# Performance work log

Hardware: AMD Instinct MI355X
Metric: run time of the kernel (lower is better)

The kernel has to match this reference:

```python
import jax, jax.numpy as jnp
import numpy as np

# sparse_shape = grid_size[::-1] + [1,0,0] for grid_size=[1408,1600,40]
Z, Y, X = 41, 1600, 1408
N = 400000
CIN, COUT = 4, 16
EPS = 1e-3  # BatchNorm1d eps from partial(nn.BatchNorm1d, eps=0.001)


def setup_inputs() -> dict:
    # unique active voxel coordinates (submanifold conv assumes no duplicates)
    rng = np.random.default_rng(0)
    pool = Z * Y * X
    raw = rng.integers(0, pool, size=3 * N, dtype=np.int64)
    lin = np.unique(raw)[:N]
    assert lin.size == N
    z = lin // (Y * X)
    rem = lin % (Y * X)
    y = rem // X
    x = rem % X
    coords = np.stack([np.zeros(N, np.int64), z, y, x], axis=1).astype(np.int32)

    key = jax.random.key(0)
    k1, k2 = jax.random.split(key)
    voxel_features = jax.random.normal(k1, (N, CIN), dtype=jnp.float32)
    # SubMConv3d weight: one [CIN,COUT] matrix per kernel offset (27 = 3^3)
    weight = jax.random.normal(k2, (27, CIN, COUT), dtype=jnp.float32) * 0.1
    gamma = jnp.ones((COUT,), dtype=jnp.float32)
    beta = jnp.zeros((COUT,), dtype=jnp.float32)
    return {
        "voxel_features": voxel_features,
        "voxel_coords": jnp.asarray(coords),
        "weight": weight,
        "gamma": gamma,
        "beta": beta,
    }


_OFFSETS = jnp.asarray(
    np.stack(np.meshgrid([-1, 0, 1], [-1, 0, 1], [-1, 0, 1], indexing="ij"), -1
             ).reshape(27, 3),
    dtype=jnp.int32,
)


def _subm_conv(feats, coords, weight):
    """Submanifold sparse 3D conv: outputs only at active voxel sites.

    Rulebook built via sorted linear keys + searchsorted (gather-GEMM).
    """
    zyx = coords[:, 1:4].astype(jnp.int32)                 # [N,3]
    keys = (zyx[:, 0] * Y + zyx[:, 1]) * X + zyx[:, 2]     # [N] unique linear key
    order = jnp.argsort(keys)
    skeys = keys[order]

    nb = zyx[None, :, :] + _OFFSETS[:, None, :]            # [27,N,3]
    inb = ((nb >= 0).all(-1)
           & (nb[..., 0] < Z) & (nb[..., 1] < Y) & (nb[..., 2] < X))
    nkeys = (nb[..., 0] * Y + nb[..., 1]) * X + nb[..., 2]  # [27,N]
    pos = jnp.clip(jnp.searchsorted(skeys, nkeys), 0, N - 1)
    found = inb & (skeys[pos] == nkeys)                    # neighbor is active
    idx = order[pos]                                       # [27,N] row into feats

    gathered = jnp.where(found[..., None], feats[idx], 0.0)  # [27,N,CIN]
    return jnp.einsum("knc,kco->no", gathered, weight)       # [N,COUT]


def reference(voxel_features, voxel_coords, weight, gamma, beta):
    out = _subm_conv(voxel_features, voxel_coords, weight)
    # BatchNorm1d in training mode: normalize over the N (voxel) axis
    mu = out.mean(0)
    var = out.var(0)
    out = (out - mu) * jax.lax.rsqrt(var + EPS) * gamma + beta
    return jax.nn.relu(out)
```

## Files before the change

### kernel.cpp

```cpp
#include <hip/hip_runtime.h>
#include <hip/hip_cooperative_groups.h>
#include <stdint.h>

namespace cg = cooperative_groups;

#define ZD 41
#define YD 1600
#define XD 1408
#define YXD (YD * XD)
#define NKEYS (ZD * YD * XD)
#define ENT_WORDS (NKEYS / 32)
#define BN_EPS 1e-3f

typedef unsigned long long u64;


__global__ void __launch_bounds__(256, 7) fused_all(
    const float4* __restrict__ feats, const int4* __restrict__ coords,
    const float* __restrict__ weight, const float* __restrict__ gamma,
    const float* __restrict__ beta, u64* __restrict__ entry,
    float* __restrict__ partial, float* __restrict__ partial2,
    float* __restrict__ out, int n, int nb, float invN) {
  cg::grid_group grid = cg::this_grid();
  const int tid = threadIdx.x;

  __shared__ float wl[27 * 64];
  __shared__ float swred[4][32];
  __shared__ float red2[8][32];
  __shared__ float redv[32];
  __shared__ float sa[16], sbv[16];

  {
    int ia = blockIdx.x * 256 + tid;
    int4 cl = coords[n - 1];
    int glast = ((cl.y * YD + cl.z) * XD + cl.w) >> 5;
    int stride = gridDim.x * 256;
    for (int g = glast + 1 + ia; g < ENT_WORDS; g += stride)
      entry[g] = (u64)(uint32_t)n;
    if (ia < n) {
      int4 c = coords[ia];
      int key = (c.y * YD + c.z) * XD + c.w;
      int g = key >> 5;
      int pkey = __shfl_up(key, 1);
      if ((tid & 63) == 0 && ia > 0) {
        int4 cp = coords[ia - 1];
        pkey = (cp.y * YD + cp.z) * XD + cp.w;
      }
      int pg = (ia > 0) ? (pkey >> 5) : -1;
      if (g != pg) {
        for (int gg = pg + 1; gg < g; ++gg) entry[gg] = (u64)(uint32_t)ia;
        uint32_t bits = 1u << (key & 31);
        int j = ia + 1;
        while (j < n) {
          int4 cj = coords[j];
          int kj = (cj.y * YD + cj.z) * XD + cj.w;
          if ((kj >> 5) != g) break;
          bits |= 1u << (kj & 31);
          ++j;
        }
        entry[g] = ((u64)bits << 32) | (uint32_t)ia;
      }
    }
  }
  __threadfence();
  grid.sync();

  for (int t = tid; t < 27 * 64; t += 256) wl[t] = weight[t];
  __syncthreads();

  int B = gridDim.x;
  int q = B >> 3, r = B & 7;
  int xcd = blockIdx.x & 7, off = blockIdx.x >> 3;
  int sbk = (xcd < r ? xcd * (q + 1) : r * (q + 1) + (xcd - r) * q) + off;
  int i = sbk * 256 + tid;

  float acc[16];
#pragma unroll
  for (int o = 0; o < 16; o++) acc[o] = 0.f;

  if (i < n) {
    int4 czyx = coords[i];
    int z = czyx.y, y = czyx.z, x = czyx.w;
    int key = (z * YD + y) * XD + x;

    {
      float4 fs = feats[i];
      const float* wp = &wl[13 * 64];
#pragma unroll
      for (int o = 0; o < 16; o++)
        acc[o] = fs.x * wp[o] + fs.y * wp[o + 16] + fs.z * wp[o + 32] +
                 fs.w * wp[o + 48];
    }

    unsigned mask27 = 0;
#pragma unroll
    for (int dzy = 0; dzy < 9; dzy++) {
      const int dz = dzy / 3 - 1, dy = dzy % 3 - 1;
      bool ok = ((unsigned)(z + dz) < (unsigned)ZD) &&
                ((unsigned)(y + dy) < (unsigned)YD);
      int base = key + dz * YXD + dy * XD - 1;
      int g0 = base >> 5;
      u64 e0 = 0, e1 = 0;
      if (ok) {
        e0 = entry[g0];
        e1 = entry[g0 + 1];
      }
      u64 W = (e0 >> 32) | (e1 & 0xFFFFFFFF00000000ull);
      unsigned m3 = (unsigned)(W >> (base & 31)) & 7u;
      mask27 |= m3 << (dzy * 3);
    }
    mask27 &= ~(1u << 13);
    if (x == 0) mask27 &= ~0x1249249u;
    if (x == XD - 1) mask27 &= ~0x4924924u;

    while (mask27) {
      int b = __ffs(mask27) - 1;
      mask27 &= mask27 - 1;
      int dzy = (b * 11) >> 5;
      int rem = b - dzy * 3;
      int dzq = (dzy * 11) >> 5;
      int dyr = dzy - dzq * 3;
      int s = key + (dzq - 1) * YXD + (dyr - 1) * XD + rem - 1;
      int gs = s >> 5;
      u64 e = entry[gs];
      int j = (int)(e & 0xFFFFFFFFull) +
              __popc((uint32_t)(e >> 32) & ((1u << (s & 31)) - 1u));
      float4 f = feats[j];
      const float* wp = &wl[b * 64];
#pragma unroll
      for (int o = 0; o < 16; o++)
        acc[o] += f.x * wp[o] + f.y * wp[o + 16] + f.z * wp[o + 32] +
                  f.w * wp[o + 48];
    }
  }

  {
    int lane = tid & 63, wv = tid >> 6;
#pragma unroll
    for (int o = 0; o < 16; o++) {
      float s = acc[o], qq = acc[o] * acc[o];
#pragma unroll
      for (int offx = 32; offx; offx >>= 1) {
        s += __shfl_xor(s, offx);
        qq += __shfl_xor(qq, offx);
      }
      if (lane == 0) {
        swred[wv][o] = s;
        swred[wv][16 + o] = qq;
      }
    }
    __syncthreads();
    if (tid < 32) {
      float v = swred[0][tid] + swred[1][tid] + swred[2][tid] + swred[3][tid];
      partial[(size_t)blockIdx.x * 32 + tid] = v;
    }
  }
  __threadfence();
  grid.sync();

  if (blockIdx.x < 64) {
    int c = tid & 31, s = tid >> 5;
    float v = 0.f;
    for (int rr = blockIdx.x + 64 * s; rr < nb; rr += 512)
      v += partial[(size_t)rr * 32 + c];
    red2[s][c] = v;
    __syncthreads();
    if (tid < 32) {
      float vv = 0.f;
#pragma unroll
      for (int k = 0; k < 8; k++) vv += red2[k][tid];
      partial2[(size_t)blockIdx.x * 32 + tid] = vv;
    }
  }
  __threadfence();
  grid.sync();

  {
    int c = tid & 31, s = tid >> 5;
    float v = 0.f;
#pragma unroll
    for (int k = 0; k < 8; k++) v += partial2[(size_t)(s + 8 * k) * 32 + c];
    red2[s][c] = v;
    __syncthreads();
    if (tid < 32) {
      float vv = 0.f;
#pragma unroll
      for (int k = 0; k < 8; k++) vv += red2[k][tid];
      redv[tid] = vv;
    }
    __syncthreads();
    if (tid < 16) {
      float mu = redv[tid] * invN;
      float var = redv[16 + tid] * invN - mu * mu;
      float inv = rsqrtf(var + BN_EPS);
      float a = gamma[tid] * inv;
      sa[tid] = a;
      sbv[tid] = beta[tid] - mu * a;
    }
    __syncthreads();
    if (i < n) {
      float4* o4 = (float4*)(out + (size_t)i * 16);
      float4 t0, t1, t2, t3;
      t0.x = fmaxf(acc[0] * sa[0] + sbv[0], 0.f);
      t0.y = fmaxf(acc[1] * sa[1] + sbv[1], 0.f);
      t0.z = fmaxf(acc[2] * sa[2] + sbv[2], 0.f);
      t0.w = fmaxf(acc[3] * sa[3] + sbv[3], 0.f);
      t1.x = fmaxf(acc[4] * sa[4] + sbv[4], 0.f);
      t1.y = fmaxf(acc[5] * sa[5] + sbv[5], 0.f);
      t1.z = fmaxf(acc[6] * sa[6] + sbv[6], 0.f);
      t1.w = fmaxf(acc[7] * sa[7] + sbv[7], 0.f);
      t2.x = fmaxf(acc[8] * sa[8] + sbv[8], 0.f);
      t2.y = fmaxf(acc[9] * sa[9] + sbv[9], 0.f);
      t2.z = fmaxf(acc[10] * sa[10] + sbv[10], 0.f);
      t2.w = fmaxf(acc[11] * sa[11] + sbv[11], 0.f);
      t3.x = fmaxf(acc[12] * sa[12] + sbv[12], 0.f);
      t3.y = fmaxf(acc[13] * sa[13] + sbv[13], 0.f);
      t3.z = fmaxf(acc[14] * sa[14] + sbv[14], 0.f);
      t3.w = fmaxf(acc[15] * sa[15] + sbv[15], 0.f);
      o4[0] = t0;
      o4[1] = t1;
      o4[2] = t2;
      o4[3] = t3;
    }
  }
}

__global__ void __launch_bounds__(256) build_index(
    const int4* __restrict__ coords, u64* __restrict__ entry, int n) {
  int i = blockIdx.x * blockDim.x + threadIdx.x;
  {
    int4 cl = coords[n - 1];
    int glast = (((cl.y * YD + cl.z) * XD + cl.w)) >> 5;
    int stride = gridDim.x * blockDim.x;
    for (int g = glast + 1 + i; g < ENT_WORDS; g += stride)
      entry[g] = (u64)(uint32_t)n;
  }
  if (i >= n) return;
  int4 c = coords[i];
  int key = (c.y * YD + c.z) * XD + c.w;
  int g = key >> 5;
  int pkey = __shfl_up(key, 1);
  if ((threadIdx.x & 63) == 0 && i > 0) {
    int4 cp = coords[i - 1];
    pkey = (cp.y * YD + cp.z) * XD + cp.w;
  }
  int pg = (i > 0) ? (pkey >> 5) : -1;
  if (g != pg) {
    for (int gg = pg + 1; gg < g; ++gg) entry[gg] = (u64)(uint32_t)i;
    uint32_t bits = 1u << (key & 31);
    int j = i + 1;
    while (j < n) {
      int4 cj = coords[j];
      int kj = (cj.y * YD + cj.z) * XD + cj.w;
      if ((kj >> 5) != g) break;
      bits |= 1u << (kj & 31);
      ++j;
    }
    entry[g] = ((u64)bits << 32) | (uint32_t)i;
  }
}

__global__ void __launch_bounds__(256) subm_conv(
    const float4* __restrict__ feats, const int4* __restrict__ coords,
    const float* __restrict__ weight, const u64* __restrict__ entry,
    float* __restrict__ out, float* __restrict__ partial, int n) {
  __shared__ float wl[27 * 64];
  __shared__ float swred[4][32];
  for (int t = threadIdx.x; t < 27 * 64; t += 256) wl[t] = weight[t];
  __syncthreads();
  int B = gridDim.x;
  int q = B >> 3, r = B & 7;
  int xcd = blockIdx.x & 7, off = blockIdx.x >> 3;
  int sb = (xcd < r ? xcd * (q + 1) : r * (q + 1) + (xcd - r) * q) + off;
  int i = sb * 256 + (int)threadIdx.x;
  float acc[16];
#pragma unroll
  for (int o = 0; o < 16; o++) acc[o] = 0.f;
  if (i < n) {
    int4 czyx = coords[i];
    int z = czyx.y, y = czyx.z, x = czyx.w;
    int key = (z * YD + y) * XD + x;
    {
      float4 fs = feats[i];
      const float* wp = &wl[13 * 64];
#pragma unroll
      for (int o = 0; o < 16; o++)
        acc[o] = fs.x * wp[o] + fs.y * wp[o + 16] + fs.z * wp[o + 32] +
                 fs.w * wp[o + 48];
    }
    unsigned mask27 = 0;
#pragma unroll
    for (int dzy = 0; dzy < 9; dzy++) {
      const int dz = dzy / 3 - 1, dy = dzy % 3 - 1;
      bool ok = ((unsigned)(z + dz) < (unsigned)ZD) &&
                ((unsigned)(y + dy) < (unsigned)YD);
      int base = key + dz * YXD + dy * XD - 1;
      int g0 = base >> 5;
      u64 e0 = 0, e1 = 0;
      if (ok) {
        e0 = entry[g0];
        e1 = entry[g0 + 1];
      }
      u64 W = (e0 >> 32) | (e1 & 0xFFFFFFFF00000000ull);
      unsigned m3 = (unsigned)(W >> (base & 31)) & 7u;
      mask27 |= m3 << (dzy * 3);
    }
    mask27 &= ~(1u << 13);
    if (x == 0) mask27 &= ~0x1249249u;
    if (x == XD - 1) mask27 &= ~0x4924924u;
    while (mask27) {
      int b = __ffs(mask27) - 1;
      mask27 &= mask27 - 1;
      int dzy = (b * 11) >> 5;
      int rem = b - dzy * 3;
      int dzq = (dzy * 11) >> 5;
      int dyr = dzy - dzq * 3;
      int s = key + (dzq - 1) * YXD + (dyr - 1) * XD + rem - 1;
      int gs = s >> 5;
      u64 e = entry[gs];
      int j = (int)(e & 0xFFFFFFFFull) +
              __popc((uint32_t)(e >> 32) & ((1u << (s & 31)) - 1u));
      float4 f = feats[j];
      const float* wp = &wl[b * 64];
#pragma unroll
      for (int o = 0; o < 16; o++)
        acc[o] += f.x * wp[o] + f.y * wp[o + 16] + f.z * wp[o + 32] +
                  f.w * wp[o + 48];
    }
    float4* o4 = (float4*)(out + (size_t)i * 16);
    o4[0] = make_float4(acc[0], acc[1], acc[2], acc[3]);
    o4[1] = make_float4(acc[4], acc[5], acc[6], acc[7]);
    o4[2] = make_float4(acc[8], acc[9], acc[10], acc[11]);
    o4[3] = make_float4(acc[12], acc[13], acc[14], acc[15]);
  }
  int lane = threadIdx.x & 63, wv = threadIdx.x >> 6;
#pragma unroll
  for (int o = 0; o < 16; o++) {
    float s = acc[o], qq = acc[o] * acc[o];
#pragma unroll
    for (int offx = 32; offx; offx >>= 1) {
      s += __shfl_xor(s, offx);
      qq += __shfl_xor(qq, offx);
    }
    if (lane == 0) {
      swred[wv][o] = s;
      swred[wv][16 + o] = qq;
    }
  }
  __syncthreads();
  if (threadIdx.x < 32) {
    float v = swred[0][threadIdx.x] + swred[1][threadIdx.x] +
              swred[2][threadIdx.x] + swred[3][threadIdx.x];
    partial[(size_t)blockIdx.x * 32 + threadIdx.x] = v;
  }
}

__global__ void __launch_bounds__(1024) bn_finalize(
    const float4* __restrict__ partial4, float* __restrict__ accum, int nb) {
  __shared__ float4 s4[1024];
  int t = threadIdx.x;
  int q = t & 7;
  int row0 = t >> 3;
  float4 v = make_float4(0.f, 0.f, 0.f, 0.f);
  for (int b = row0; b < nb; b += 128) {
    float4 p = partial4[(size_t)b * 8 + q];
    v.x += p.x;
    v.y += p.y;
    v.z += p.z;
    v.w += p.w;
  }
  s4[t] = v;
  __syncthreads();
  for (int half = 64; half >= 1; half >>= 1) {
    if (row0 < half) {
      float4 o = s4[t + half * 8];
      v.x += o.x;
      v.y += o.y;
      v.z += o.z;
      v.w += o.w;
      s4[t] = v;
    }
    __syncthreads();
  }
  if (t < 8) ((float4*)accum)[t] = s4[t];
}

__global__ void __launch_bounds__(256) bn_apply(
    float* __restrict__ out, const float* __restrict__ accum,
    const float* __restrict__ gamma, const float* __restrict__ beta, int n4,
    float invN) {
  __shared__ float sa[16], sb[16];
  int t = threadIdx.x;
  if (t < 16) {
    float mu = accum[t] * invN;
    float var = accum[16 + t] * invN - mu * mu;
    float inv = rsqrtf(var + BN_EPS);
    float a = gamma[t] * inv;
    sa[t] = a;
    sb[t] = beta[t] - mu * a;
  }
  __syncthreads();
  int i = blockIdx.x * 256 + t;
  if (i >= n4) return;
  float4* p = (float4*)out;
  float4 v = p[i];
  int c0 = (i & 3) * 4;
  v.x = fmaxf(v.x * sa[c0 + 0] + sb[c0 + 0], 0.f);
  v.y = fmaxf(v.y * sa[c0 + 1] + sb[c0 + 1], 0.f);
  v.z = fmaxf(v.z * sa[c0 + 2] + sb[c0 + 2], 0.f);
  v.w = fmaxf(v.w * sa[c0 + 3] + sb[c0 + 3], 0.f);
  p[i] = v;
}

extern "C" void kernel_launch(void* const* d_in, const int* in_sizes, int n_in,
                              void* d_out, int out_size, void* d_ws,
                              size_t ws_size, hipStream_t stream) {
  const float4* feats = (const float4*)d_in[0];
  const int4* coords = (const int4*)d_in[1];
  const float* weight = (const float*)d_in[2];
  const float* gamma = (const float*)d_in[3];
  const float* beta = (const float*)d_in[4];
  int n = in_sizes[0] / 4;

  float* accum = (float*)d_ws;
  u64* entry = (u64*)((char*)d_ws + 256);
  float* partial = (float*)((char*)d_ws + 256 + (size_t)ENT_WORDS * 8 + 16);
  int nb = (n + 255) / 256;
  float* partial2 = partial + (size_t)nb * 32;
  float* out = (float*)d_out;
  float invN = 1.0f / n;

  int maxB = 0, numCU = 0;
  hipOccupancyMaxActiveBlocksPerMultiprocessor(&maxB, fused_all, 256, 0);
  hipDeviceGetAttribute(&numCU, hipDeviceAttributeMultiprocessorCount, 0);

  if ((long)maxB * numCU >= nb) {
    void* args[] = {(void*)&feats, (void*)&coords,  (void*)&weight,
                    (void*)&gamma, (void*)&beta,    (void*)&entry,
                    (void*)&partial, (void*)&partial2, (void*)&out,
                    (void*)&n,     (void*)&nb,      (void*)&invN};
    hipLaunchCooperativeKernel((void*)fused_all, dim3(nb), dim3(256), args, 0,
                               stream);
  } else {
    hipLaunchKernelGGL(build_index, dim3(nb), dim3(256), 0, stream, coords,
                       entry, n);
    hipLaunchKernelGGL(subm_conv, dim3(nb), dim3(256), 0, stream, feats,
                       coords, weight, entry, out, partial, n);
    hipLaunchKernelGGL(bn_finalize, dim3(1), dim3(1024), 0, stream,
                       (const float4*)partial, accum, nb);
    int n4 = n * 4;
    hipLaunchKernelGGL(bn_apply, dim3((n4 + 255) / 256), dim3(256), 0, stream,
                       out, accum, gamma, beta, n4, invN);
  }
}
```

Measured before the change: 124.3 us.

## Fix cooperative grid at 1024 blocks with two voxels per thread

```diff
diff --git a/kernel.cpp b/kernel.cpp
--- a/kernel.cpp
+++ b/kernel.cpp
@@ -11,126 +11,135 @@
 #define NKEYS (ZD * YD * XD)
 #define ENT_WORDS (NKEYS / 32)
 #define BN_EPS 1e-3f
+#define GRIDB 1024
+#define TOT (GRIDB * 256)
 
 typedef unsigned long long u64;
 
 
-__global__ void __launch_bounds__(256, 7) fused_all(
+__global__ void __launch_bounds__(256, 4) fused_all(
     const float4* __restrict__ feats, const int4* __restrict__ coords,
     const float* __restrict__ weight, const float* __restrict__ gamma,
     const float* __restrict__ beta, u64* __restrict__ entry,
     float* __restrict__ partial, float* __restrict__ partial2,
-    float* __restrict__ out, int n, int nb, float invN) {
+    float* __restrict__ out, int n, float invN) {
   cg::grid_group grid = cg::this_grid();
   const int tid = threadIdx.x;
 
-  __shared__ float wl[27 * 64];
+  __shared__ float wl[27 * 68];
   __shared__ float swred[4][32];
   __shared__ float red2[8][32];
   __shared__ float redv[32];
   __shared__ float sa[16], sbv[16];
 
   {
-    int ia = blockIdx.x * 256 + tid;
     int4 cl = coords[n - 1];
     int glast = ((cl.y * YD + cl.z) * XD + cl.w) >> 5;
-    int stride = gridDim.x * 256;
-    for (int g = glast + 1 + ia; g < ENT_WORDS; g += stride)
+    int base = blockIdx.x * 256 + tid;
+    for (int g = glast + 1 + base; g < ENT_WORDS; g += TOT)
       entry[g] = (u64)(uint32_t)n;
-    if (ia < n) {
-      int4 c = coords[ia];
-      int key = (c.y * YD + c.z) * XD + c.w;
-      int g = key >> 5;
-      int pkey = __shfl_up(key, 1);
-      if ((tid & 63) == 0 && ia > 0) {
-        int4 cp = coords[ia - 1];
-        pkey = (cp.y * YD + cp.z) * XD + cp.w;
-      }
-      int pg = (ia > 0) ? (pkey >> 5) : -1;
-      if (g != pg) {
-        for (int gg = pg + 1; gg < g; ++gg) entry[gg] = (u64)(uint32_t)ia;
-        uint32_t bits = 1u << (key & 31);
-        int j = ia + 1;
-        while (j < n) {
-          int4 cj = coords[j];
-          int kj = (cj.y * YD + cj.z) * XD + cj.w;
-          if ((kj >> 5) != g) break;
-          bits |= 1u << (kj & 31);
-          ++j;
+#pragma unroll
+    for (int pass = 0; pass < 2; pass++) {
+      int ia = pass * TOT + base;
+      if (ia < n) {
+        int4 c = coords[ia];
+        int key = (c.y * YD + c.z) * XD + c.w;
+        int g = key >> 5;
+        int pkey = __shfl_up(key, 1);
+        if ((tid & 63) == 0 && ia > 0) {
+          int4 cp = coords[ia - 1];
+          pkey = (cp.y * YD + cp.z) * XD + cp.w;
         }
-        entry[g] = ((u64)bits << 32) | (uint32_t)ia;
+        int pg = (ia > 0) ? (pkey >> 5) : -1;
+        if (g != pg) {
+          for (int gg = pg + 1; gg < g; ++gg) entry[gg] = (u64)(uint32_t)ia;
+          uint32_t bits = 1u << (key & 31);
+          int j = ia + 1;
+          while (j < n) {
+            int4 cj = coords[j];
+            int kj = (cj.y * YD + cj.z) * XD + cj.w;
+            if ((kj >> 5) != g) break;
+            bits |= 1u << (kj & 31);
+            ++j;
+          }
+          entry[g] = ((u64)bits << 32) | (uint32_t)ia;
+        }
       }
     }
   }
   __threadfence();
   grid.sync();
 
-  for (int t = tid; t < 27 * 64; t += 256) wl[t] = weight[t];
+  for (int t = tid; t < 27 * 64; t += 256)
+    wl[(t >> 6) * 68 + (t & 63)] = weight[t];
   __syncthreads();
 
-  int B = gridDim.x;
-  int q = B >> 3, r = B & 7;
-  int xcd = blockIdx.x & 7, off = blockIdx.x >> 3;
-  int sbk = (xcd < r ? xcd * (q + 1) : r * (q + 1) + (xcd - r) * q) + off;
-  int i = sbk * 256 + tid;
-
-  float acc[16];
-#pragma unroll
-  for (int o = 0; o < 16; o++) acc[o] = 0.f;
-
-  if (i < n) {
-    int4 czyx = coords[i];
-    int z = czyx.y, y = czyx.z, x = czyx.w;
-    int key = (z * YD + y) * XD + x;
-
-    {
-      float4 fs = feats[i];
-      const float* wp = &wl[13 * 64];
-#pragma unroll
-      for (int o = 0; o < 16; o++)
-        acc[o] = fs.x * wp[o] + fs.y * wp[o + 16] + fs.z * wp[o + 32] +
-                 fs.w * wp[o + 48];
-    }
-
-    unsigned mask27 = 0;
-#pragma unroll
-    for (int dzy = 0; dzy < 9; dzy++) {
-      const int dz = dzy / 3 - 1, dy = dzy % 3 - 1;
-      bool ok = ((unsigned)(z + dz) < (unsigned)ZD) &&
-                ((unsigned)(y + dy) < (unsigned)YD);
-      int base = key + dz * YXD + dy * XD - 1;
-      int g0 = base >> 5;
-      u64 e0 = 0, e1 = 0;
-      if (ok) {
-        e0 = entry[g0];
-        e1 = entry[g0 + 1];
-      }
-      u64 W = (e0 >> 32) | (e1 & 0xFFFFFFFF00000000ull);
-      unsigned m3 = (unsigned)(W >> (base & 31)) & 7u;
-      mask27 |= m3 << (dzy * 3);
-    }
-    mask27 &= ~(1u << 13);
-    if (x == 0) mask27 &= ~0x1249249u;
-    if (x == XD - 1) mask27 &= ~0x4924924u;
-
-    while (mask27) {
-      int b = __ffs(mask27) - 1;
-      mask27 &= mask27 - 1;
-      int dzy = (b * 11) >> 5;
-      int rem = b - dzy * 3;
-      int dzq = (dzy * 11) >> 5;
-      int dyr = dzy - dzq * 3;
-      int s = key + (dzq - 1) * YXD + (dyr - 1) * XD + rem - 1;
-      int gs = s >> 5;
-      u64 e = entry[gs];
-      int j = (int)(e & 0xFFFFFFFFull) +
-              __popc((uint32_t)(e >> 32) & ((1u << (s & 31)) - 1u));
-      float4 f = feats[j];
-      const float* wp = &wl[b * 64];
-#pragma unroll
-      for (int o = 0; o < 16; o++)
-        acc[o] += f.x * wp[o] + f.y * wp[o + 16] + f.z * wp[o + 32] +
-                  f.w * wp[o + 48];
+  int sbk = (blockIdx.x & 7) * (GRIDB / 8) + (blockIdx.x >> 3);
+  const int v0 = sbk * 256 + tid;
+
+  float acc[2][16];
+#pragma unroll
+  for (int rp = 0; rp < 2; rp++)
+#pragma unroll
+    for (int o = 0; o < 16; o++) acc[rp][o] = 0.f;
+
+#pragma unroll
+  for (int rp = 0; rp < 2; rp++) {
+    int i = v0 + rp * TOT;
+    if (i < n) {
+      int4 czyx = coords[i];
+      int z = czyx.y, y = czyx.z, x = czyx.w;
+      int key = (z * YD + y) * XD + x;
+
+      {
+        float4 fs = feats[i];
+        const float* wp = &wl[13 * 68];
+#pragma unroll
+        for (int o = 0; o < 16; o++)
+          acc[rp][o] = fs.x * wp[o] + fs.y * wp[o + 16] + fs.z * wp[o + 32] +
+                       fs.w * wp[o + 48];
+      }
+
+      unsigned mask27 = 0;
+#pragma unroll
+      for (int dzy = 0; dzy < 9; dzy++) {
+        const int dz = dzy / 3 - 1, dy = dzy % 3 - 1;
+        bool ok = ((unsigned)(z + dz) < (unsigned)ZD) &&
+                  ((unsigned)(y + dy) < (unsigned)YD);
+        int base = key + dz * YXD + dy * XD - 1;
+        int g0 = base >> 5;
+        u64 e0 = 0, e1 = 0;
+        if (ok) {
+          e0 = entry[g0];
+          e1 = entry[g0 + 1];
+        }
+        u64 W = (e0 >> 32) | (e1 & 0xFFFFFFFF00000000ull);
+        unsigned m3 = (unsigned)(W >> (base & 31)) & 7u;
+        mask27 |= m3 << (dzy * 3);
+      }
+      mask27 &= ~(1u << 13);
+      if (x == 0) mask27 &= ~0x1249249u;
+      if (x == XD - 1) mask27 &= ~0x4924924u;
+
+      while (mask27) {
+        int b = __ffs(mask27) - 1;
+        mask27 &= mask27 - 1;
+        int dzy = (b * 11) >> 5;
+        int rem = b - dzy * 3;
+        int dzq = (dzy * 11) >> 5;
+        int dyr = dzy - dzq * 3;
+        int s = key + (dzq - 1) * YXD + (dyr - 1) * XD + rem - 1;
+        int gs = s >> 5;
+        u64 e = entry[gs];
+        int j = (int)(e & 0xFFFFFFFFull) +
+                __popc((uint32_t)(e >> 32) & ((1u << (s & 31)) - 1u));
+        float4 f = feats[j];
+        const float* wp = &wl[b * 68];
+#pragma unroll
+        for (int o = 0; o < 16; o++)
+          acc[rp][o] += f.x * wp[o] + f.y * wp[o + 16] + f.z * wp[o + 32] +
+                        f.w * wp[o + 48];
+      }
     }
   }
 
@@ -138,7 +147,8 @@
     int lane = tid & 63, wv = tid >> 6;
 #pragma unroll
     for (int o = 0; o < 16; o++) {
-      float s = acc[o], qq = acc[o] * acc[o];
+      float s = acc[0][o] + acc[1][o];
+      float qq = acc[0][o] * acc[0][o] + acc[1][o] * acc[1][o];
 #pragma unroll
       for (int offx = 32; offx; offx >>= 1) {
         s += __shfl_xor(s, offx);
@@ -161,7 +171,7 @@
   if (blockIdx.x < 64) {
     int c = tid & 31, s = tid >> 5;
     float v = 0.f;
-    for (int rr = blockIdx.x + 64 * s; rr < nb; rr += 512)
+    for (int rr = blockIdx.x + 64 * s; rr < GRIDB; rr += 512)
       v += partial[(size_t)rr * 32 + c];
     red2[s][c] = v;
     __syncthreads();
@@ -198,29 +208,33 @@
       sbv[tid] = beta[tid] - mu * a;
     }
     __syncthreads();
-    if (i < n) {
-      float4* o4 = (float4*)(out + (size_t)i * 16);
-      float4 t0, t1, t2, t3;
-      t0.x = fmaxf(acc[0] * sa[0] + sbv[0], 0.f);
-      t0.y = fmaxf(acc[1] * sa[1] + sbv[1], 0.f);
-      t0.z = fmaxf(acc[2] * sa[2] + sbv[2], 0.f);
-      t0.w = fmaxf(acc[3] * sa[3] + sbv[3], 0.f);
-      t1.x = fmaxf(acc[4] * sa[4] + sbv[4], 0.f);
-      t1.y = fmaxf(acc[5] * sa[5] + sbv[5], 0.f);
-      t1.z = fmaxf(acc[6] * sa[6] + sbv[6], 0.f);
-      t1.w = fmaxf(acc[7] * sa[7] + sbv[7], 0.f);
-      t2.x = fmaxf(acc[8] * sa[8] + sbv[8], 0.f);
-      t2.y = fmaxf(acc[9] * sa[9] + sbv[9], 0.f);
-      t2.z = fmaxf(acc[10] * sa[10] + sbv[10], 0.f);
-      t2.w = fmaxf(acc[11] * sa[11] + sbv[11], 0.f);
-      t3.x = fmaxf(acc[12] * sa[12] + sbv[12], 0.f);
-      t3.y = fmaxf(acc[13] * sa[13] + sbv[13], 0.f);
-      t3.z = fmaxf(acc[14] * sa[14] + sbv[14], 0.f);
-      t3.w = fmaxf(acc[15] * sa[15] + sbv[15], 0.f);
-      o4[0] = t0;
-      o4[1] = t1;
-      o4[2] = t2;
-      o4[3] = t3;
+#pragma unroll
+    for (int rp = 0; rp < 2; rp++) {
+      int i = v0 + rp * TOT;
+      if (i < n) {
+        float4* o4 = (float4*)(out + (size_t)i * 16);
+        float4 t0, t1, t2, t3;
+        t0.x = fmaxf(acc[rp][0] * sa[0] + sbv[0], 0.f);
+        t0.y = fmaxf(acc[rp][1] * sa[1] + sbv[1], 0.f);
+        t0.z = fmaxf(acc[rp][2] * sa[2] + sbv[2], 0.f);
+        t0.w = fmaxf(acc[rp][3] * sa[3] + sbv[3], 0.f);
+        t1.x = fmaxf(acc[rp][4] * sa[4] + sbv[4], 0.f);
+        t1.y = fmaxf(acc[rp][5] * sa[5] + sbv[5], 0.f);
+        t1.z = fmaxf(acc[rp][6] * sa[6] + sbv[6], 0.f);
+        t1.w = fmaxf(acc[rp][7] * sa[7] + sbv[7], 0.f);
+        t2.x = fmaxf(acc[rp][8] * sa[8] + sbv[8], 0.f);
+        t2.y = fmaxf(acc[rp][9] * sa[9] + sbv[9], 0.f);
+        t2.z = fmaxf(acc[rp][10] * sa[10] + sbv[10], 0.f);
+        t2.w = fmaxf(acc[rp][11] * sa[11] + sbv[11], 0.f);
+        t3.x = fmaxf(acc[rp][12] * sa[12] + sbv[12], 0.f);
+        t3.y = fmaxf(acc[rp][13] * sa[13] + sbv[13], 0.f);
+        t3.z = fmaxf(acc[rp][14] * sa[14] + sbv[14], 0.f);
+        t3.w = fmaxf(acc[rp][15] * sa[15] + sbv[15], 0.f);
+        o4[0] = t0;
+        o4[1] = t1;
+        o4[2] = t2;
+        o4[3] = t3;
+      }
     }
   }
 }
@@ -425,8 +439,8 @@
   float* accum = (float*)d_ws;
   u64* entry = (u64*)((char*)d_ws + 256);
   float* partial = (float*)((char*)d_ws + 256 + (size_t)ENT_WORDS * 8 + 16);
-  int nb = (n + 255) / 256;
-  float* partial2 = partial + (size_t)nb * 32;
+  int nbF = (n + 255) / 256;
+  float* partial2 = partial + (size_t)nbF * 32;
   float* out = (float*)d_out;
   float invN = 1.0f / n;
 
@@ -434,20 +448,20 @@
   hipOccupancyMaxActiveBlocksPerMultiprocessor(&maxB, fused_all, 256, 0);
   hipDeviceGetAttribute(&numCU, hipDeviceAttributeMultiprocessorCount, 0);
 
-  if ((long)maxB * numCU >= nb) {
-    void* args[] = {(void*)&feats, (void*)&coords,  (void*)&weight,
-                    (void*)&gamma, (void*)&beta,    (void*)&entry,
+  if ((long)maxB * numCU >= GRIDB && (long)TOT * 2 >= n) {
+    void* args[] = {(void*)&feats,   (void*)&coords, (void*)&weight,
+                    (void*)&gamma,   (void*)&beta,   (void*)&entry,
                     (void*)&partial, (void*)&partial2, (void*)&out,
-                    (void*)&n,     (void*)&nb,      (void*)&invN};
-    hipLaunchCooperativeKernel((void*)fused_all, dim3(nb), dim3(256), args, 0,
-                               stream);
+                    (void*)&n,       (void*)&invN};
+    hipLaunchCooperativeKernel((void*)fused_all, dim3(GRIDB), dim3(256), args,
+                               0, stream);
   } else {
-    hipLaunchKernelGGL(build_index, dim3(nb), dim3(256), 0, stream, coords,
+    hipLaunchKernelGGL(build_index, dim3(nbF), dim3(256), 0, stream, coords,
                        entry, n);
-    hipLaunchKernelGGL(subm_conv, dim3(nb), dim3(256), 0, stream, feats,
+    hipLaunchKernelGGL(subm_conv, dim3(nbF), dim3(256), 0, stream, feats,
                        coords, weight, entry, out, partial, n);
     hipLaunchKernelGGL(bn_finalize, dim3(1), dim3(1024), 0, stream,
-                       (const float4*)partial, accum, nb);
+                       (const float4*)partial, accum, nbF);
     int n4 = n * 4;
     hipLaunchKernelGGL(bn_apply, dim3((n4 + 255) / 256), dim3(256), 0, stream,
                        out, accum, gamma, beta, n4, invN);
```

Result: no change. 125.0 us (+0.6%).
